# Kernel optimization log

Measured on AMD Instinct MI355X. Metric: run time of the kernel, lower is better.

Reference implementation:

```python
import jax, jax.numpy as jnp
import numpy as np

D = 300  # feature dim hardcoded in the layer
L = 50   # headline length (e = ones(50))
B = 16384


def setup_inputs() -> dict:
    key = jax.random.key(0)
    ks = jax.random.split(key, 7)
    s = 0.05  # keras initializations.get('normal') uses scale=0.05
    return {
        "Y": jax.random.normal(ks[0], (B, D, L), dtype=jnp.float32),
        "h_n": jax.random.normal(ks[1], (B, D), dtype=jnp.float32),
        "W_y": s * jax.random.normal(ks[2], (D, D), dtype=jnp.float32),
        "W_h": s * jax.random.normal(ks[3], (D, D), dtype=jnp.float32),
        "W_p": s * jax.random.normal(ks[4], (D, D), dtype=jnp.float32),
        "W_x": s * jax.random.normal(ks[5], (D, D), dtype=jnp.float32),
        "w": s * jax.random.normal(ks[6], (D,), dtype=jnp.float32),
    }


def reference(Y, h_n, W_y, W_h, W_p, W_x, w):
    # M = tanh(W_y Y + (W_h h_n) e^T)   -> [B, D, L]
    Wh_h = jnp.einsum('de,be->bd', W_h, h_n)            # [B, D]
    M = jnp.tanh(jnp.einsum('de,bel->bdl', W_y, Y) + Wh_h[:, :, None])
    # alpha = softmax(w^T M) over headline positions    -> [B, L]
    alpha = jax.nn.softmax(jnp.einsum('d,bdl->bl', w, M), axis=-1)
    # r = Y alpha^T                                      -> [B, D]
    r = jnp.einsum('bdl,bl->bd', Y, alpha)
    # h* = tanh(W_p r + W_x h_n)                         -> [B, D]
    h = jnp.tanh(jnp.einsum('de,be->bd', W_p, r) + jnp.einsum('de,be->bd', W_x, h_n))
    return h
```

## Files before the change

kernel.cpp:

```cpp
#include <hip/hip_runtime.h>
#include <hip/hip_bf16.h>

typedef __attribute__((ext_vector_type(8))) short bf16x8;
typedef __attribute__((ext_vector_type(4))) float f32x4;
typedef unsigned short u16;
typedef unsigned int u32;

__device__ __forceinline__ u16 f2bf(float f){
    u32 u; __builtin_memcpy(&u,&f,4);
    u = (u + 0x7FFFu + ((u>>16)&1u)) >> 16;
    return (u16)u;
}
__device__ __forceinline__ float bf2f(u16 h){
    u32 u = ((u32)h)<<16; float f; __builtin_memcpy(&f,&u,4); return f;
}
__device__ __forceinline__ u32 pkbf(float a, float b){
    __hip_bfloat162 h = __float22bfloat162_rn(float2{a,b});
    u32 r; __builtin_memcpy(&r,&h,4); return r;
}
__device__ __forceinline__ float fast_tanh(float x){
    float e = __builtin_amdgcn_exp2f(x * 2.8853900817779268f);
    return 1.f - 2.f*__builtin_amdgcn_rcpf(e + 1.f);
}
__device__ __forceinline__ float wval(const float* W, int d, int e){
    return (d<300 && e<300) ? W[d*300+e] : 0.f;
}

__global__ void k_prep(const float* __restrict__ Wy, const float* __restrict__ Wh,
                       const float* __restrict__ Wp, const float* __restrict__ Wx,
                       const float* __restrict__ w,
                       u16* __restrict__ wy_swz, u16* __restrict__ wh_swz,
                       u16* __restrict__ wpx_swz, float* __restrict__ w_pad)
{
    int gid = blockIdx.x*256 + threadIdx.x;
    if (gid < 320) w_pad[gid] = (gid < 300) ? w[gid] : 0.f;
    u16* dst; const float* A; const float* Bm = nullptr; int t, nks;
    if (gid < 12800)      { dst = wy_swz;  t = gid;        nks = 10; A = Wy; }
    else if (gid < 25600) { dst = wh_swz;  t = gid-12800;  nks = 10; A = Wh; }
    else                  { dst = wpx_swz; t = gid-25600;  nks = 20; A = Wp; Bm = Wx; }
    int ks   = (t/64) % nks;
    int tile = t/(nks*64);
    int lane = t & 63;
    int d  = tile*16 + (lane & 15);
    int kb = ks*32 + (lane>>4)*8;
    u32 pk[4];
    #pragma unroll
    for (int jj=0; jj<4; jj++){
        int k0 = kb + 2*jj, k1 = k0 + 1;
        float v0, v1;
        if (Bm){ v0 = (k0 < 320) ? wval(A,d,k0) : wval(Bm,d,k0-320);
                 v1 = (k1 < 320) ? wval(A,d,k1) : wval(Bm,d,k1-320); }
        else   { v0 = wval(A,d,k0); v1 = wval(A,d,k1); }
        pk[jj] = (u32)f2bf(v0) | ((u32)f2bf(v1) << 16);
    }
    uint4 u; u.x = pk[0]; u.y = pk[1]; u.z = pk[2]; u.w = pk[3];
    ((uint4*)dst)[t] = u;
}

__global__ __launch_bounds__(256,3) void k_whh(const float* __restrict__ hn,
        const u16* __restrict__ wh_swz, u16* __restrict__ whh)
{
    __shared__ __align__(16) u16 A[64*328];
    int tid = threadIdx.x;
    int rb = blockIdx.x >> 1, half = blockIdx.x & 1;
    int m0 = rb*64;
    for (int i = tid; i < 9600; i += 256){
        int r = i/150, c = (i%150)*2;
        float2 v = *(const float2*)(hn + (size_t)(m0+r)*300 + c);
        *(u32*)&A[r*328 + c] = pkbf(v.x, v.y);
    }
    for (int i = tid; i < 64*14; i += 256){ int r = i/14, c = 300 + (i%14)*2; *(u32*)&A[r*328+c] = 0; }
    __syncthreads();
    int w = tid>>6, lane = tid&63, lo = lane&15, hi = lane>>4;
    f32x4 acc[10];
    #pragma unroll
    for (int t=0; t<10; t++) acc[t] = (f32x4){0.f,0.f,0.f,0.f};
    const bf16x8* wsz = (const bf16x8*)wh_swz;
    for (int ks=0; ks<10; ks++){
        bf16x8 aF = *(const bf16x8*)&A[(w*16+lo)*328 + ks*32 + hi*8];
        #pragma unroll
        for (int t=0; t<10; t++){
            int nt = half*10 + t;
            bf16x8 bF = wsz[(nt*10+ks)*64 + lane];
            acc[t] = __builtin_amdgcn_mfma_f32_16x16x32_bf16(aF, bF, acc[t], 0,0,0);
        }
    }
    #pragma unroll
    for (int t=0; t<10; t++)
      #pragma unroll
      for (int rg=0; rg<4; rg++){
        int m = m0 + w*16 + hi*4 + rg;
        whh[(size_t)m*320 + (half*10+t)*16 + lo] = f2bf(acc[t][rg]);
      }
}

__global__ __launch_bounds__(256,4) void k_attn(const float* __restrict__ Y,
        const u16* __restrict__ whh, const u16* __restrict__ wy_swz,
        const float* __restrict__ w_pad, u16* __restrict__ r_out)
{
    __shared__ __align__(16) u16 Ylds[50*328];
    __shared__ float whh_s[320];
    __shared__ float w_s[320];
    __shared__ float s_red[4][64];
    __shared__ float alpha_s[64];
    char* Yb8 = (char*)Ylds;
    int tid = threadIdx.x;
    int b = blockIdx.x;
    int w = tid>>6, lane = tid&63, lo = lane&15, hi = lane>>4;
    const float* Yb = Y + (size_t)b*15000;
    const float C2L = 2.8853900817779268f;

#define STAGE_TASK(T) do{                                                     \
        int e4 = (T)/12, l4 = ((T)%12)*4;                                     \
        const float* p0 = Yb + e4*200 + l4;                                   \
        float4 r0 = *(const float4*)p0;                                       \
        float2 r1a = *(const float2*)(p0+50), r1b = *(const float2*)(p0+52);  \
        float4 r2 = *(const float4*)(p0+100);                                 \
        float2 r3a = *(const float2*)(p0+150), r3b = *(const float2*)(p0+152);\
        float e0v[4]={r0.x,r0.y,r0.z,r0.w};                                   \
        float e1v[4]={r1a.x,r1a.y,r1b.x,r1b.y};                               \
        float e2v[4]={r2.x,r2.y,r2.z,r2.w};                                   \
        float e3v[4]={r3a.x,r3a.y,r3b.x,r3b.y};                               \
        _Pragma("unroll")                                                     \
        for (int j=0;j<4;j++){                                                \
            int row = l4+j;                                                   \
            uint2 uu; uu.x = pkbf(e0v[j], e1v[j]); uu.y = pkbf(e2v[j], e3v[j]);\
            *(uint2*)(Yb8 + row*656 + e4*8) = uu;                             \
        } }while(0)

    {
        #pragma unroll
        for (int it=0; it<3; it++){ int t = tid + it*256; STAGE_TASK(t); }
        if (tid < 132){ int t = tid + 768; STAGE_TASK(t); }
    }
#undef STAGE_TASK
    if (tid < 75){
        int e4 = tid;
        const float* p0 = Yb + e4*200;
        float2 a0 = *(const float2*)(p0+48);
        float2 a1 = *(const float2*)(p0+98);
        float2 a2 = *(const float2*)(p0+148);
        float2 a3 = *(const float2*)(p0+198);
        uint2 u48; u48.x = pkbf(a0.x, a1.x); u48.y = pkbf(a2.x, a3.x);
        uint2 u49; u49.x = pkbf(a0.y, a1.y); u49.y = pkbf(a2.y, a3.y);
        *(uint2*)(Yb8 + 48*656 + e4*8) = u48;
        *(uint2*)(Yb8 + 49*656 + e4*8) = u49;
    }
    if (tid < 250){
        int row = tid/5, q = tid%5;
        uint2 z; z.x = 0; z.y = 0;
        *(uint2*)(Yb8 + row*656 + 600 + q*8) = z;
    }
    for (int i = tid; i < 160; i += 256){
        u32 z = *(const u32*)&whh[(size_t)b*320 + 2*i];
        whh_s[2*i]   = bf2f((u16)(z & 0xffff));
        whh_s[2*i+1] = bf2f((u16)(z >> 16));
    }
    for (int i = tid; i < 320; i += 256) w_s[i] = w_pad[i];
    __syncthreads();

    const bf16x8* wyf = (const bf16x8*)wy_swz;
    float sp[4] = {0.f,0.f,0.f,0.f};
    float swd = 0.f;
    int rb_[4];
    #pragma unroll
    for (int c=0;c<4;c++){ int row=c*16+lo; if (row>=50) row-=48; rb_[c]=row*656; }
    int hi16 = hi*16;

#define GEMM_PASS(Q0, NQ)                                                      \
    {                                                                          \
        f32x4 acc[NQ][4];                                                      \
        _Pragma("unroll") for (int q=0;q<NQ;q++)                               \
            _Pragma("unroll") for (int c=0;c<4;c++)                            \
                acc[q][c] = (f32x4){0.f,0.f,0.f,0.f};                          \
        bf16x8 A0[NQ], A1[NQ], B0[4], B1[4];                                   \
        _Pragma("unroll") for (int q=0;q<NQ;q++)                               \
            A0[q] = wyf[((w+4*((Q0)+q))*10)*64 + lane];                        \
        _Pragma("unroll") for (int c=0;c<4;c++)                                \
            B0[c] = *(const bf16x8*)(Yb8 + rb_[c] + hi16);                     \
        _Pragma("unroll 1")                                                    \
        for (int kk=0; kk<5; kk++){                                            \
            int k1 = 2*kk+1, k2 = 2*kk+2;                                      \
            int k2c = (k2 < 10) ? k2 : 0;                                      \
            _Pragma("unroll") for (int q=0;q<NQ;q++)                           \
                A1[q] = wyf[((w+4*((Q0)+q))*10 + k1)*64 + lane];               \
            _Pragma("unroll") for (int c=0;c<4;c++)                            \
                B1[c] = *(const bf16x8*)(Yb8 + rb_[c] + k1*64 + hi16);         \
            _Pragma("unroll") for (int q=0;q<NQ;q++)                           \
                _Pragma("unroll") for (int c=0;c<4;c++)                        \
                    acc[q][c] = __builtin_amdgcn_mfma_f32_16x16x32_bf16(       \
                        A0[q], B0[c], acc[q][c], 0,0,0);                       \
            _Pragma("unroll") for (int q=0;q<NQ;q++)                           \
                A0[q] = wyf[((w+4*((Q0)+q))*10 + k2)*64 + lane];               \
            _Pragma("unroll") for (int c=0;c<4;c++)                            \
                B0[c] = *(const bf16x8*)(Yb8 + rb_[c] + k2c*64 + hi16);        \
            _Pragma("unroll") for (int q=0;q<NQ;q++)                           \
                _Pragma("unroll") for (int c=0;c<4;c++)                        \
                    acc[q][c] = __builtin_amdgcn_mfma_f32_16x16x32_bf16(       \
                        A1[q], B1[c], acc[q][c], 0,0,0);                       \
        }                                                                      \
        _Pragma("unroll") for (int q=0;q<NQ;q++)                               \
            _Pragma("unroll") for (int rg=0;rg<4;rg++){                        \
                int d = (w + 4*((Q0)+q))*16 + hi*4 + rg;                       \
                float wh = whh_s[d], wd_ = w_s[d];                             \
                float whc = wh*C2L, wd2n = -2.f*wd_;                           \
                swd += wd_;                                                    \
                _Pragma("unroll") for (int c=0;c<4;c++){                       \
                    float targ = __builtin_fmaf(acc[q][c][rg], C2L, whc);      \
                    float e2x  = __builtin_amdgcn_exp2f(targ);                 \
                    float rc   = __builtin_amdgcn_rcpf(e2x + 1.f);             \
                    sp[c] = __builtin_fmaf(wd2n, rc, sp[c]);                   \
                }                                                              \
            }                                                                  \
    }

    GEMM_PASS(0, 3)
    GEMM_PASS(3, 2)
#undef GEMM_PASS

    #pragma unroll
    for (int c=0;c<4;c++){
        sp[c] += swd;
        sp[c] += __shfl_xor(sp[c], 16);
        sp[c] += __shfl_xor(sp[c], 32);
    }
    if (lane < 16){
        #pragma unroll
        for (int c=0;c<4;c++) s_red[w][c*16 + lane] = sp[c];
    }
    __syncthreads();

    if (w == 0){
        float sv = (lane < 50)
            ? (s_red[0][lane] + s_red[1][lane] + s_red[2][lane] + s_red[3][lane])
            : -1e30f;
        float mx = sv;
        #pragma unroll
        for (int off=32; off; off>>=1) mx = fmaxf(mx, __shfl_xor(mx, off));
        float pv = (lane < 50) ? __builtin_amdgcn_exp2f((sv - mx)*1.4426950408889634f) : 0.f;
        float sm = pv;
        #pragma unroll
        for (int off=32; off; off>>=1) sm += __shfl_xor(sm, off);
        alpha_s[lane] = pv * __builtin_amdgcn_rcpf(sm);
    }
    __syncthreads();

    if (tid < 160){
        float r0 = 0.f, r1 = 0.f;
        if (tid < 150){
            #pragma unroll 10
            for (int l=0; l<50; l++){
                u32 z = *(const u32*)(Yb8 + l*656 + tid*4);
                float a_ = alpha_s[l];
                r0 += a_ * bf2f((u16)(z & 0xffff));
                r1 += a_ * bf2f((u16)(z >> 16));
            }
        }
        *(u32*)&r_out[(size_t)b*320 + 2*tid] = pkbf(r0, r1);
    }
}

__global__ __launch_bounds__(256,3) void k_out(const u16* __restrict__ r_in,
        const float* __restrict__ hn, const u16* __restrict__ wpx_swz,
        float* __restrict__ out)
{
    __shared__ __align__(16) u16 A[32*648];
    int tid = threadIdx.x;
    int m0 = blockIdx.x*32;
    for (int i = tid; i < 32*40; i += 256){
        int r = i/40, c8 = (i%40)*8;
        uint4 v = *(const uint4*)&r_in[(size_t)(m0+r)*320 + c8];
        *(uint4*)&A[r*648 + c8] = v;
    }
    for (int i = tid; i < 32*150; i += 256){
        int r = i/150, c = (i%150)*2;
        float2 v = *(const float2*)(hn + (size_t)(m0+r)*300 + c);
        *(u32*)&A[r*648 + 320 + c] = pkbf(v.x, v.y);
    }
    for (int i = tid; i < 32*14; i += 256){ int r = i/14, c = 620 + (i%14)*2; *(u32*)&A[r*648+c] = 0; }
    __syncthreads();
    int w = tid>>6, lane = tid&63, lo = lane&15, hi = lane>>4;
    int wm = w & 1, wn = w >> 1;
    f32x4 acc[10];
    #pragma unroll
    for (int t=0; t<10; t++) acc[t] = (f32x4){0.f,0.f,0.f,0.f};
    const bf16x8* wsz = (const bf16x8*)wpx_swz;
    for (int ks=0; ks<20; ks++){
        bf16x8 aF = *(const bf16x8*)&A[(wm*16+lo)*648 + ks*32 + hi*8];
        #pragma unroll
        for (int t=0; t<10; t++){
            int nt = wn*10 + t;
            bf16x8 bF = wsz[(nt*20+ks)*64 + lane];
            acc[t] = __builtin_amdgcn_mfma_f32_16x16x32_bf16(aF, bF, acc[t], 0,0,0);
        }
    }
    #pragma unroll
    for (int t=0; t<10; t++){
        int n = (wn*10+t)*16 + lo;
        if (n < 300){
            #pragma unroll
            for (int rg=0; rg<4; rg++){
                int m = m0 + wm*16 + hi*4 + rg;
                out[(size_t)m*300 + n] = fast_tanh(acc[t][rg]);
            }
        }
    }
}

extern "C" void kernel_launch(void* const* d_in, const int* in_sizes, int n_in,
                              void* d_out, int out_size, void* d_ws, size_t ws_size,
                              hipStream_t stream)
{
    const float* Y  = (const float*)d_in[0];
    const float* hn = (const float*)d_in[1];
    const float* Wy = (const float*)d_in[2];
    const float* Wh = (const float*)d_in[3];
    const float* Wp = (const float*)d_in[4];
    const float* Wx = (const float*)d_in[5];
    const float* w  = (const float*)d_in[6];
    int B = in_sizes[1] / 300;

    char* ws = (char*)d_ws;
    u16*   wy_swz  = (u16*)(ws + 0);
    u16*   wh_swz  = (u16*)(ws + 204800);
    u16*   wpx_swz = (u16*)(ws + 409600);
    float* w_pad   = (float*)(ws + 819200);
    u16*   whh     = (u16*)(ws + 820480);
    u16*   r_ws    = (u16*)(ws + 820480 + (size_t)B*640);

    k_prep<<<200, 256, 0, stream>>>(Wy, Wh, Wp, Wx, w, wy_swz, wh_swz, wpx_swz, w_pad);
    k_whh <<<(B/64)*2, 256, 0, stream>>>(hn, wh_swz, whh);
    k_attn<<<B, 256, 0, stream>>>(Y, whh, wy_swz, w_pad, r_ws);
    k_out <<<B/32, 256, 0, stream>>>(r_ws, hn, wpx_swz, (float*)d_out);
}
```

Measured before the change: 507.4 us.

## Widen attention kernel to 1024 threads and split GEMM across 16 waves

Measured after the change: 485.6 us. 4.3% less time.

```diff
diff --git a/kernel.cpp b/kernel.cpp
--- a/kernel.cpp
+++ b/kernel.cpp
@@ -94,118 +94,94 @@
       }
 }
 
-__global__ __launch_bounds__(256,4) void k_attn(const float* __restrict__ Y,
+__global__ __launch_bounds__(1024) void k_attn(const float* __restrict__ Y,
         const u16* __restrict__ whh, const u16* __restrict__ wy_swz,
         const float* __restrict__ w_pad, u16* __restrict__ r_out)
 {
     __shared__ __align__(16) u16 Ylds[50*328];
     __shared__ float whh_s[320];
     __shared__ float w_s[320];
-    __shared__ float s_red[4][64];
+    __shared__ float s_red[8][64];
     __shared__ float alpha_s[64];
+
+    const int tid = threadIdx.x;
+    const int wv = tid>>6, lane = tid&63, lo = lane&15, hi = lane>>4;
+    const int wd = wv>>1, wc = wv&1;
+    const int hi16 = hi*16;
+    const int b = blockIdx.x;
     char* Yb8 = (char*)Ylds;
-    int tid = threadIdx.x;
-    int b = blockIdx.x;
-    int w = tid>>6, lane = tid&63, lo = lane&15, hi = lane>>4;
-    const float* Yb = Y + (size_t)b*15000;
     const float C2L = 2.8853900817779268f;
 
-#define STAGE_TASK(T) do{                                                     \
-        int e4 = (T)/12, l4 = ((T)%12)*4;                                     \
-        const float* p0 = Yb + e4*200 + l4;                                   \
-        float4 r0 = *(const float4*)p0;                                       \
-        float2 r1a = *(const float2*)(p0+50), r1b = *(const float2*)(p0+52);  \
-        float4 r2 = *(const float4*)(p0+100);                                 \
-        float2 r3a = *(const float2*)(p0+150), r3b = *(const float2*)(p0+152);\
-        float e0v[4]={r0.x,r0.y,r0.z,r0.w};                                   \
-        float e1v[4]={r1a.x,r1a.y,r1b.x,r1b.y};                               \
-        float e2v[4]={r2.x,r2.y,r2.z,r2.w};                                   \
-        float e3v[4]={r3a.x,r3a.y,r3b.x,r3b.y};                               \
-        _Pragma("unroll")                                                     \
-        for (int j=0;j<4;j++){                                                \
-            int row = l4+j;                                                   \
-            uint2 uu; uu.x = pkbf(e0v[j], e1v[j]); uu.y = pkbf(e2v[j], e3v[j]);\
-            *(uint2*)(Yb8 + row*656 + e4*8) = uu;                             \
-        } }while(0)
-
-    {
-        #pragma unroll
-        for (int it=0; it<3; it++){ int t = tid + it*256; STAGE_TASK(t); }
-        if (tid < 132){ int t = tid + 768; STAGE_TASK(t); }
-    }
-#undef STAGE_TASK
-    if (tid < 75){
-        int e4 = tid;
-        const float* p0 = Yb + e4*200;
-        float2 a0 = *(const float2*)(p0+48);
-        float2 a1 = *(const float2*)(p0+98);
-        float2 a2 = *(const float2*)(p0+148);
-        float2 a3 = *(const float2*)(p0+198);
-        uint2 u48; u48.x = pkbf(a0.x, a1.x); u48.y = pkbf(a2.x, a3.x);
-        uint2 u49; u49.x = pkbf(a0.y, a1.y); u49.y = pkbf(a2.y, a3.y);
-        *(uint2*)(Yb8 + 48*656 + e4*8) = u48;
-        *(uint2*)(Yb8 + 49*656 + e4*8) = u49;
-    }
-    if (tid < 250){
-        int row = tid/5, q = tid%5;
-        uint2 z; z.x = 0; z.y = 0;
-        *(uint2*)(Yb8 + row*656 + 600 + q*8) = z;
-    }
-    for (int i = tid; i < 160; i += 256){
+    int rb_[2];
+    { int r0 = (2*wc)*16 + lo;   if (r0>=50) r0-=48; rb_[0]=r0*656;
+      int r1 = (2*wc+1)*16 + lo; if (r1>=50) r1-=48; rb_[1]=r1*656; }
+
+    for (int i = tid; i < 320; i += 1024) w_s[i] = w_pad[i];
+    for (int i = tid; i < 700; i += 1024){
+        int row = i/14, c2 = 150 + i%14;
+        *(u32*)(Yb8 + row*656 + c2*4) = 0;
+    }
+    for (int i = tid; i < 160; i += 1024){
         u32 z = *(const u32*)&whh[(size_t)b*320 + 2*i];
         whh_s[2*i]   = bf2f((u16)(z & 0xffff));
         whh_s[2*i+1] = bf2f((u16)(z >> 16));
     }
-    for (int i = tid; i < 320; i += 256) w_s[i] = w_pad[i];
+    {
+        const float* gb_ = Y + (size_t)b*15000;
+        #pragma unroll
+        for (int it=0; it<4; it++){
+            int t = tid + it*1024;
+            if (t < 3750){
+                int e2 = t/25, l2 = t%25;
+                const float* p_ = gb_ + e2*100 + 2*l2;
+                float2 sA = *(const float2*)p_;
+                float2 sB = *(const float2*)(p_ + 50);
+                *(u32*)(Yb8 + (2*l2)*656   + e2*4) = pkbf(sA.x, sB.x);
+                *(u32*)(Yb8 + (2*l2+1)*656 + e2*4) = pkbf(sA.y, sB.y);
+            }
+        }
+    }
     __syncthreads();
 
     const bf16x8* wyf = (const bf16x8*)wy_swz;
-    float sp[4] = {0.f,0.f,0.f,0.f};
+    float sp[2] = {0.f,0.f};
     float swd = 0.f;
-    int rb_[4];
-    #pragma unroll
-    for (int c=0;c<4;c++){ int row=c*16+lo; if (row>=50) row-=48; rb_[c]=row*656; }
-    int hi16 = hi*16;
-
-#define GEMM_PASS(Q0, NQ)                                                      \
+#define GEMM_BODY(NT)                                                          \
     {                                                                          \
-        f32x4 acc[NQ][4];                                                      \
-        _Pragma("unroll") for (int q=0;q<NQ;q++)                               \
-            _Pragma("unroll") for (int c=0;c<4;c++)                            \
-                acc[q][c] = (f32x4){0.f,0.f,0.f,0.f};                          \
-        bf16x8 A0[NQ], A1[NQ], B0[4], B1[4];                                   \
-        _Pragma("unroll") for (int q=0;q<NQ;q++)                               \
-            A0[q] = wyf[((w+4*((Q0)+q))*10)*64 + lane];                        \
-        _Pragma("unroll") for (int c=0;c<4;c++)                                \
-            B0[c] = *(const bf16x8*)(Yb8 + rb_[c] + hi16);                     \
+        f32x4 acc[NT][2];                                                      \
+        _Pragma("unroll") for (int q=0;q<NT;q++){                              \
+            acc[q][0]=(f32x4){0.f,0.f,0.f,0.f};                                \
+            acc[q][1]=(f32x4){0.f,0.f,0.f,0.f}; }                              \
+        bf16x8 A0[NT], A1[NT], B0[2], B1[2];                                   \
+        _Pragma("unroll") for (int q=0;q<NT;q++)                               \
+            A0[q] = wyf[((wd+8*q)*10)*64 + lane];                              \
+        B0[0] = *(const bf16x8*)(Yb8 + rb_[0] + hi16);                         \
+        B0[1] = *(const bf16x8*)(Yb8 + rb_[1] + hi16);                         \
         _Pragma("unroll 1")                                                    \
         for (int kk=0; kk<5; kk++){                                            \
-            int k1 = 2*kk+1, k2 = 2*kk+2;                                      \
-            int k2c = (k2 < 10) ? k2 : 0;                                      \
-            _Pragma("unroll") for (int q=0;q<NQ;q++)                           \
-                A1[q] = wyf[((w+4*((Q0)+q))*10 + k1)*64 + lane];               \
-            _Pragma("unroll") for (int c=0;c<4;c++)                            \
-                B1[c] = *(const bf16x8*)(Yb8 + rb_[c] + k1*64 + hi16);         \
-            _Pragma("unroll") for (int q=0;q<NQ;q++)                           \
-                _Pragma("unroll") for (int c=0;c<4;c++)                        \
-                    acc[q][c] = __builtin_amdgcn_mfma_f32_16x16x32_bf16(       \
-                        A0[q], B0[c], acc[q][c], 0,0,0);                       \
-            _Pragma("unroll") for (int q=0;q<NQ;q++)                           \
-                A0[q] = wyf[((w+4*((Q0)+q))*10 + k2)*64 + lane];               \
-            _Pragma("unroll") for (int c=0;c<4;c++)                            \
-                B0[c] = *(const bf16x8*)(Yb8 + rb_[c] + k2c*64 + hi16);        \
-            _Pragma("unroll") for (int q=0;q<NQ;q++)                           \
-                _Pragma("unroll") for (int c=0;c<4;c++)                        \
-                    acc[q][c] = __builtin_amdgcn_mfma_f32_16x16x32_bf16(       \
-                        A1[q], B1[c], acc[q][c], 0,0,0);                       \
+            int k1 = 2*kk+1, k2 = (2*kk+2<10)?(2*kk+2):0;                      \
+            _Pragma("unroll") for (int q=0;q<NT;q++)                           \
+                A1[q] = wyf[((wd+8*q)*10 + k1)*64 + lane];                     \
+            B1[0] = *(const bf16x8*)(Yb8 + rb_[0] + k1*64 + hi16);             \
+            B1[1] = *(const bf16x8*)(Yb8 + rb_[1] + k1*64 + hi16);             \
+            _Pragma("unroll") for (int q=0;q<NT;q++){                          \
+                acc[q][0] = __builtin_amdgcn_mfma_f32_16x16x32_bf16(A0[q],B0[0],acc[q][0],0,0,0); \
+                acc[q][1] = __builtin_amdgcn_mfma_f32_16x16x32_bf16(A0[q],B0[1],acc[q][1],0,0,0); } \
+            _Pragma("unroll") for (int q=0;q<NT;q++)                           \
+                A0[q] = wyf[((wd+8*q)*10 + k2)*64 + lane];                     \
+            B0[0] = *(const bf16x8*)(Yb8 + rb_[0] + k2*64 + hi16);             \
+            B0[1] = *(const bf16x8*)(Yb8 + rb_[1] + k2*64 + hi16);             \
+            _Pragma("unroll") for (int q=0;q<NT;q++){                          \
+                acc[q][0] = __builtin_amdgcn_mfma_f32_16x16x32_bf16(A1[q],B1[0],acc[q][0],0,0,0); \
+                acc[q][1] = __builtin_amdgcn_mfma_f32_16x16x32_bf16(A1[q],B1[1],acc[q][1],0,0,0); } \
         }                                                                      \
-        _Pragma("unroll") for (int q=0;q<NQ;q++)                               \
+        _Pragma("unroll") for (int q=0;q<NT;q++)                               \
             _Pragma("unroll") for (int rg=0;rg<4;rg++){                        \
-                int d = (w + 4*((Q0)+q))*16 + hi*4 + rg;                       \
+                int d = (wd+8*q)*16 + hi*4 + rg;                               \
                 float wh = whh_s[d], wd_ = w_s[d];                             \
                 float whc = wh*C2L, wd2n = -2.f*wd_;                           \
                 swd += wd_;                                                    \
-                _Pragma("unroll") for (int c=0;c<4;c++){                       \
+                _Pragma("unroll") for (int c=0;c<2;c++){                       \
                     float targ = __builtin_fmaf(acc[q][c][rg], C2L, whc);      \
                     float e2x  = __builtin_amdgcn_exp2f(targ);                 \
                     float rc   = __builtin_amdgcn_rcpf(e2x + 1.f);             \
@@ -213,27 +189,27 @@
                 }                                                              \
             }                                                                  \
     }
-
-    GEMM_PASS(0, 3)
-    GEMM_PASS(3, 2)
-#undef GEMM_PASS
-
-    #pragma unroll
-    for (int c=0;c<4;c++){
+    if (wd < 3) { GEMM_BODY(3) } else { GEMM_BODY(2) }
+#undef GEMM_BODY
+    #pragma unroll
+    for (int c=0;c<2;c++){
         sp[c] += swd;
         sp[c] += __shfl_xor(sp[c], 16);
         sp[c] += __shfl_xor(sp[c], 32);
     }
     if (lane < 16){
-        #pragma unroll
-        for (int c=0;c<4;c++) s_red[w][c*16 + lane] = sp[c];
-    }
-    __syncthreads();
-
-    if (w == 0){
-        float sv = (lane < 50)
-            ? (s_red[0][lane] + s_red[1][lane] + s_red[2][lane] + s_red[3][lane])
-            : -1e30f;
+        s_red[wd][(2*wc+0)*16 + lane] = sp[0];
+        s_red[wd][(2*wc+1)*16 + lane] = sp[1];
+    }
+    __syncthreads();
+
+    if (wv == 0){
+        float sv = -1e30f;
+        if (lane < 50){
+            sv = 0.f;
+            #pragma unroll
+            for (int k=0;k<8;k++) sv += s_red[k][lane];
+        }
         float mx = sv;
         #pragma unroll
         for (int off=32; off; off>>=1) mx = fmaxf(mx, __shfl_xor(mx, off));
@@ -252,8 +228,8 @@
             for (int l=0; l<50; l++){
                 u32 z = *(const u32*)(Yb8 + l*656 + tid*4);
                 float a_ = alpha_s[l];
-                r0 += a_ * bf2f((u16)(z & 0xffff));
-                r1 += a_ * bf2f((u16)(z >> 16));
+                r0 = __builtin_fmaf(a_, bf2f((u16)(z & 0xffff)), r0);
+                r1 = __builtin_fmaf(a_, bf2f((u16)(z >> 16)),   r1);
             }
         }
         *(u32*)&r_out[(size_t)b*320 + 2*tid] = pkbf(r0, r1);
@@ -330,6 +306,6 @@
 
     k_prep<<<200, 256, 0, stream>>>(Wy, Wh, Wp, Wx, w, wy_swz, wh_swz, wpx_swz, w_pad);
     k_whh <<<(B/64)*2, 256, 0, stream>>>(hn, wh_swz, whh);
-    k_attn<<<B, 256, 0, stream>>>(Y, whh, wy_swz, w_pad, r_ws);
+    k_attn<<<B, 1024, 0, stream>>>(Y, whh, wy_swz, w_pad, r_ws);
     k_out <<<B/32, 256, 0, stream>>>(r_ws, hn, wpx_swz, (float*)d_out);
 }
```
